# Kernel optimization log

Measured on AMD Instinct MI355X. Metric: run time of the kernel, lower is better.

Reference implementation:

```python
import jax, jax.numpy as jnp
import numpy as np

TOTAL_TOKENS = 131072
D_MODEL = 1024
NUM_SEGS = 64


def setup_inputs() -> dict:
    key = jax.random.key(0)
    k1, k2, k3 = jax.random.split(key, 3)
    x = jax.random.normal(k1, (TOTAL_TOKENS, D_MODEL), dtype=jnp.float32)
    # strictly increasing interior boundaries -> no empty segments
    interior = np.sort(np.random.default_rng(0).choice(
        np.arange(1, TOTAL_TOKENS), size=NUM_SEGS - 1, replace=False))
    cu_seqlens = jnp.asarray(np.concatenate([[0], interior, [TOTAL_TOKENS]]),
                             dtype=jnp.int32)
    W = jax.random.normal(k2, (D_MODEL, 1), dtype=jnp.float32) * (D_MODEL ** -0.5)
    b = jnp.zeros((1,), dtype=jnp.float32)
    return {"x": x, "cu_seqlens": cu_seqlens, "W": W, "b": b}


def reference(x, cu_seqlens, W, b):
    total = x.shape[0]
    num_segs = cu_seqlens.shape[0] - 1
    # token -> segment id
    seg_ids = jnp.searchsorted(cu_seqlens, jnp.arange(total, dtype=cu_seqlens.dtype),
                               side="right") - 1  # [T]
    # attention scores: Linear(d_model, 1)
    scores = (x @ W + b)[:, 0]  # [T]
    # segment-wise numerically stable softmax
    seg_max = jax.ops.segment_max(scores, seg_ids, num_segments=num_segs)  # [B]
    p = jnp.exp(scores - seg_max[seg_ids])  # [T]
    seg_sum = jax.ops.segment_sum(p, seg_ids, num_segments=num_segs)  # [B]
    w = p / seg_sum[seg_ids]  # [T]
    # softmax-weighted sum per segment -> [B, D]
    out = jax.ops.segment_sum(x * w[:, None], seg_ids, num_segments=num_segs)
    return out
```

## Files before the change

### kernel.cpp

```cpp
#include <hip/hip_runtime.h>
#include <math.h>

#define D_MODEL 1024
#define NUM_SEGS 64
#define CT 64
#define TOTAL_TOKENS 131072
#define MAXC (TOTAL_TOKENS / CT + NUM_SEGS)
#define WAVES_PER_BLOCK 4

__global__ __launch_bounds__(256) void seg_pool_pass1(
    const float* __restrict__ x, const int* __restrict__ cu,
    const float* __restrict__ W, const float* __restrict__ bias_p,
    float* __restrict__ m_arr, float* __restrict__ l_arr,
    float* __restrict__ o_arr)
{
    __shared__ int s_cu[NUM_SEGS + 1];
    __shared__ int s_cuc[NUM_SEGS + 1];

    const int tid = threadIdx.x;
    if (tid <= NUM_SEGS) s_cu[tid] = cu[tid];
    __syncthreads();
    if (tid == 0) {
        int acc = 0;
        s_cuc[0] = 0;
        for (int s = 0; s < NUM_SEGS; ++s) {
            acc += (s_cu[s + 1] - s_cu[s] + CT - 1) / CT;
            s_cuc[s + 1] = acc;
        }
    }
    __syncthreads();

    const int wave = tid >> 6;
    const int lane = tid & 63;
    const int chunk = blockIdx.x * WAVES_PER_BLOCK + wave;
    const int total_chunks = s_cuc[NUM_SEGS];
    if (chunk >= total_chunks) return;

    int lo = 0, hi = NUM_SEGS;
    while (hi - lo > 1) {
        int mid = (lo + hi) >> 1;
        if (s_cuc[mid] <= chunk) lo = mid; else hi = mid;
    }
    const int seg = lo;
    const int t0 = s_cu[seg] + (chunk - s_cuc[seg]) * CT;
    const int t1 = min(t0 + CT, s_cu[seg + 1]);

    float4 w4[4];
#pragma unroll
    for (int k = 0; k < 4; ++k)
        w4[k] = *(const float4*)(W + k * 256 + lane * 4);
    const float bias = bias_p[0];

    float m = -INFINITY;
    float lsum = 0.0f;
    float4 o[4];
#pragma unroll
    for (int k = 0; k < 4; ++k) o[k] = make_float4(0.f, 0.f, 0.f, 0.f);

    for (int t = t0; t < t1; ++t) {
        const float* row = x + (size_t)t * D_MODEL;
        float4 v[4];
#pragma unroll
        for (int k = 0; k < 4; ++k)
            v[k] = *(const float4*)(row + k * 256 + lane * 4);

        float dot = 0.0f;
#pragma unroll
        for (int k = 0; k < 4; ++k) {
            dot += v[k].x * w4[k].x;
            dot += v[k].y * w4[k].y;
            dot += v[k].z * w4[k].z;
            dot += v[k].w * w4[k].w;
        }
#pragma unroll
        for (int off = 32; off > 0; off >>= 1)
            dot += __shfl_xor(dot, off, 64);

        const float sc = dot + bias;
        const float mnew = fmaxf(m, sc);
        const float scale = __expf(m - mnew);
        const float p = __expf(sc - mnew);
        lsum = lsum * scale + p;
#pragma unroll
        for (int k = 0; k < 4; ++k) {
            o[k].x = o[k].x * scale + p * v[k].x;
            o[k].y = o[k].y * scale + p * v[k].y;
            o[k].z = o[k].z * scale + p * v[k].z;
            o[k].w = o[k].w * scale + p * v[k].w;
        }
        m = mnew;
    }

    if (lane == 0) { m_arr[chunk] = m; l_arr[chunk] = lsum; }
    float* op = o_arr + (size_t)chunk * D_MODEL;
#pragma unroll
    for (int k = 0; k < 4; ++k)
        *(float4*)(op + k * 256 + lane * 4) = o[k];
}

__global__ __launch_bounds__(256) void seg_pool_pass2(
    const int* __restrict__ cu,
    const float* __restrict__ m_arr, const float* __restrict__ l_arr,
    const float* __restrict__ o_arr, float* __restrict__ out)
{
    __shared__ int s_cu[NUM_SEGS + 1];
    __shared__ int s_cuc[NUM_SEGS + 1];

    const int tid = threadIdx.x;
    if (tid <= NUM_SEGS) s_cu[tid] = cu[tid];
    __syncthreads();
    if (tid == 0) {
        int acc = 0;
        s_cuc[0] = 0;
        for (int s = 0; s < NUM_SEGS; ++s) {
            acc += (s_cu[s + 1] - s_cu[s] + CT - 1) / CT;
            s_cuc[s + 1] = acc;
        }
    }
    __syncthreads();

    const int seg = blockIdx.x;
    const int c0 = s_cuc[seg], c1 = s_cuc[seg + 1];

    float mstar = -INFINITY;
    for (int c = c0; c < c1; ++c) mstar = fmaxf(mstar, m_arr[c]);

    float4 acc = make_float4(0.f, 0.f, 0.f, 0.f);
    float lstar = 0.0f;
    for (int c = c0; c < c1; ++c) {
        const float sc = __expf(m_arr[c] - mstar);
        lstar += sc * l_arr[c];
        const float4 oc = *(const float4*)(o_arr + (size_t)c * D_MODEL + tid * 4);
        acc.x += sc * oc.x;
        acc.y += sc * oc.y;
        acc.z += sc * oc.z;
        acc.w += sc * oc.w;
    }
    const float inv = 1.0f / lstar;
    acc.x *= inv; acc.y *= inv; acc.z *= inv; acc.w *= inv;
    *(float4*)(out + (size_t)seg * D_MODEL + tid * 4) = acc;
}

extern "C" void kernel_launch(void* const* d_in, const int* in_sizes, int n_in,
                              void* d_out, int out_size, void* d_ws, size_t ws_size,
                              hipStream_t stream) {
    const float* x  = (const float*)d_in[0];
    const int*   cu = (const int*)d_in[1];
    const float* W  = (const float*)d_in[2];
    const float* b  = (const float*)d_in[3];
    float* out = (float*)d_out;

    float* m_arr = (float*)d_ws;
    float* l_arr = m_arr + MAXC;
    float* o_arr = l_arr + MAXC;

    const int blocks1 = (MAXC + WAVES_PER_BLOCK - 1) / WAVES_PER_BLOCK;
    seg_pool_pass1<<<dim3(blocks1), dim3(256), 0, stream>>>(
        x, cu, W, b, m_arr, l_arr, o_arr);
    seg_pool_pass2<<<dim3(NUM_SEGS), dim3(256), 0, stream>>>(
        cu, m_arr, l_arr, o_arr, out);
}
```

Measured before the change: 751.8 us.

## Shrink chunks, precompute chunk table in setup kernel, widen pass2 grid

```diff
diff --git a/kernel.cpp b/kernel.cpp
--- a/kernel.cpp
+++ b/kernel.cpp
@@ -3,47 +3,56 @@
 
 #define D_MODEL 1024
 #define NUM_SEGS 64
-#define CT 64
+#define CT 16
 #define TOTAL_TOKENS 131072
 #define MAXC (TOTAL_TOKENS / CT + NUM_SEGS)
-#define WAVES_PER_BLOCK 4
+#define WPB 4
 
-__global__ __launch_bounds__(256) void seg_pool_pass1(
-    const float* __restrict__ x, const int* __restrict__ cu,
-    const float* __restrict__ W, const float* __restrict__ bias_p,
-    float* __restrict__ m_arr, float* __restrict__ l_arr,
-    float* __restrict__ o_arr)
+__global__ __launch_bounds__(256) void seg_pool_setup(
+    const int* __restrict__ cu, int* __restrict__ cuc_out,
+    int2* __restrict__ ctab)
 {
     __shared__ int s_cu[NUM_SEGS + 1];
     __shared__ int s_cuc[NUM_SEGS + 1];
-
     const int tid = threadIdx.x;
     if (tid <= NUM_SEGS) s_cu[tid] = cu[tid];
     __syncthreads();
     if (tid == 0) {
-        int acc = 0;
-        s_cuc[0] = 0;
+        int acc = 0; s_cuc[0] = 0;
         for (int s = 0; s < NUM_SEGS; ++s) {
             acc += (s_cu[s + 1] - s_cu[s] + CT - 1) / CT;
             s_cuc[s + 1] = acc;
         }
     }
     __syncthreads();
+    if (tid <= NUM_SEGS) cuc_out[tid] = s_cuc[tid];
+    const int total = s_cuc[NUM_SEGS];
+    for (int i = tid; i < MAXC; i += 256) {
+        int2 e;
+        if (i >= total) { e.x = 0; e.y = 0; }
+        else {
+            int lo = 0, hi = NUM_SEGS;
+            while (hi - lo > 1) {
+                int mid = (lo + hi) >> 1;
+                if (s_cuc[mid] <= i) lo = mid; else hi = mid;
+            }
+            e.x = s_cu[lo] + (i - s_cuc[lo]) * CT;
+            e.y = min(e.x + CT, s_cu[lo + 1]);
+        }
+        ctab[i] = e;
+    }
+}
 
-    const int wave = tid >> 6;
-    const int lane = tid & 63;
-    const int chunk = blockIdx.x * WAVES_PER_BLOCK + wave;
-    const int total_chunks = s_cuc[NUM_SEGS];
-    if (chunk >= total_chunks) return;
-
-    int lo = 0, hi = NUM_SEGS;
-    while (hi - lo > 1) {
-        int mid = (lo + hi) >> 1;
-        if (s_cuc[mid] <= chunk) lo = mid; else hi = mid;
-    }
-    const int seg = lo;
-    const int t0 = s_cu[seg] + (chunk - s_cuc[seg]) * CT;
-    const int t1 = min(t0 + CT, s_cu[seg + 1]);
+__global__ __launch_bounds__(256) void seg_pool_pass1(
+    const float* __restrict__ x, const int2* __restrict__ ctab,
+    const float* __restrict__ W, const float* __restrict__ bias_p,
+    float* __restrict__ m_arr, float* __restrict__ l_arr,
+    float* __restrict__ o_arr)
+{
+    const int wave = threadIdx.x >> 6;
+    const int lane = threadIdx.x & 63;
+    const int chunk = blockIdx.x * WPB + wave;
+    const int2 r = ctab[chunk];
 
     float4 w4[4];
 #pragma unroll
@@ -57,7 +66,7 @@
 #pragma unroll
     for (int k = 0; k < 4; ++k) o[k] = make_float4(0.f, 0.f, 0.f, 0.f);
 
-    for (int t = t0; t < t1; ++t) {
+    for (int t = r.x; t < r.y; ++t) {
         const float* row = x + (size_t)t * D_MODEL;
         float4 v[4];
 #pragma unroll
@@ -67,10 +76,8 @@
         float dot = 0.0f;
 #pragma unroll
         for (int k = 0; k < 4; ++k) {
-            dot += v[k].x * w4[k].x;
-            dot += v[k].y * w4[k].y;
-            dot += v[k].z * w4[k].z;
-            dot += v[k].w * w4[k].w;
+            dot += v[k].x * w4[k].x; dot += v[k].y * w4[k].y;
+            dot += v[k].z * w4[k].z; dot += v[k].w * w4[k].w;
         }
 #pragma unroll
         for (int off = 32; off > 0; off >>= 1)
@@ -99,46 +106,25 @@
 }
 
 __global__ __launch_bounds__(256) void seg_pool_pass2(
-    const int* __restrict__ cu,
-    const float* __restrict__ m_arr, const float* __restrict__ l_arr,
-    const float* __restrict__ o_arr, float* __restrict__ out)
+    const int* __restrict__ cuc, const float* __restrict__ m_arr,
+    const float* __restrict__ l_arr, const float* __restrict__ o_arr,
+    float* __restrict__ out)
 {
-    __shared__ int s_cu[NUM_SEGS + 1];
-    __shared__ int s_cuc[NUM_SEGS + 1];
-
-    const int tid = threadIdx.x;
-    if (tid <= NUM_SEGS) s_cu[tid] = cu[tid];
-    __syncthreads();
-    if (tid == 0) {
-        int acc = 0;
-        s_cuc[0] = 0;
-        for (int s = 0; s < NUM_SEGS; ++s) {
-            acc += (s_cu[s + 1] - s_cu[s] + CT - 1) / CT;
-            s_cuc[s + 1] = acc;
-        }
-    }
-    __syncthreads();
-
     const int seg = blockIdx.x;
-    const int c0 = s_cuc[seg], c1 = s_cuc[seg + 1];
+    const int c0 = cuc[seg], c1 = cuc[seg + 1];
+    const int d = blockIdx.y * 256 + threadIdx.x;
 
     float mstar = -INFINITY;
     for (int c = c0; c < c1; ++c) mstar = fmaxf(mstar, m_arr[c]);
 
-    float4 acc = make_float4(0.f, 0.f, 0.f, 0.f);
-    float lstar = 0.0f;
+    float acc = 0.0f, lstar = 0.0f;
+#pragma unroll 4
     for (int c = c0; c < c1; ++c) {
-        const float sc = __expf(m_arr[c] - mstar);
-        lstar += sc * l_arr[c];
-        const float4 oc = *(const float4*)(o_arr + (size_t)c * D_MODEL + tid * 4);
-        acc.x += sc * oc.x;
-        acc.y += sc * oc.y;
-        acc.z += sc * oc.z;
-        acc.w += sc * oc.w;
+        const float coef = __expf(m_arr[c] - mstar);
+        lstar += coef * l_arr[c];
+        acc += coef * o_arr[(size_t)c * D_MODEL + d];
     }
-    const float inv = 1.0f / lstar;
-    acc.x *= inv; acc.y *= inv; acc.z *= inv; acc.w *= inv;
-    *(float4*)(out + (size_t)seg * D_MODEL + tid * 4) = acc;
+    out[(size_t)seg * D_MODEL + d] = acc / lstar;
 }
 
 extern "C" void kernel_launch(void* const* d_in, const int* in_sizes, int n_in,
@@ -150,13 +136,16 @@
     const float* b  = (const float*)d_in[3];
     float* out = (float*)d_out;
 
-    float* m_arr = (float*)d_ws;
-    float* l_arr = m_arr + MAXC;
-    float* o_arr = l_arr + MAXC;
+    char* w = (char*)d_ws;
+    int2* ctab  = (int2*)w;                       w += (size_t)MAXC * 8;
+    int*  cuc   = (int*)w;                        w += 80 * 4;
+    float* m_arr = (float*)w;                     w += (size_t)MAXC * 4;
+    float* l_arr = (float*)w;                     w += (size_t)MAXC * 4;
+    float* o_arr = (float*)w;
 
-    const int blocks1 = (MAXC + WAVES_PER_BLOCK - 1) / WAVES_PER_BLOCK;
-    seg_pool_pass1<<<dim3(blocks1), dim3(256), 0, stream>>>(
-        x, cu, W, b, m_arr, l_arr, o_arr);
-    seg_pool_pass2<<<dim3(NUM_SEGS), dim3(256), 0, stream>>>(
-        cu, m_arr, l_arr, o_arr, out);
+    seg_pool_setup<<<dim3(1), dim3(256), 0, stream>>>(cu, cuc, ctab);
+    seg_pool_pass1<<<dim3(MAXC / WPB), dim3(256), 0, stream>>>(
+        x, ctab, W, b, m_arr, l_arr, o_arr);
+    seg_pool_pass2<<<dim3(NUM_SEGS, 4), dim3(256), 0, stream>>>(
+        cuc, m_arr, l_arr, o_arr, out);
 }
```

Measured after the change: 829.8 us. 1.1x slower.
